# Performance work log

Hardware: AMD Instinct MI355X
Metric: run time of the kernel (lower is better)

The kernel has to match this reference:

```python
import jax, jax.numpy as jnp
import numpy as np

EMB_DIM = 256
HEAD_DIM = 32


def setup_inputs() -> dict:
    key = jax.random.key(0)
    kx, kq, kk, kv = jax.random.split(key, 4)
    B, S = 4, 4096
    x = jax.random.normal(kx, (B, S, EMB_DIM), dtype=jnp.float32)
    # Linear(emb_dim, head_dim, bias=False): store as [emb_dim, head_dim]
    sc = 1.0 / np.sqrt(EMB_DIM)
    Wq = jax.random.normal(kq, (EMB_DIM, HEAD_DIM), dtype=jnp.float32) * sc
    Wk = jax.random.normal(kk, (EMB_DIM, HEAD_DIM), dtype=jnp.float32) * sc
    Wv = jax.random.normal(kv, (EMB_DIM, HEAD_DIM), dtype=jnp.float32) * sc
    return {"x": x, "Wq": Wq, "Wk": Wk, "Wv": Wv}


def reference(x, Wq, Wk, Wv):
    # single-head attention with POST-softmax scaling (as in source).
    # Dropout treated as identity (eval mode) for determinism.
    scaling = HEAD_DIM ** (-0.5)
    q = jnp.einsum('bse,ed->bsd', x, Wq)
    k = jnp.einsum('bse,ed->bsd', x, Wk)
    v = jnp.einsum('bse,ed->bsd', x, Wv)
    energy = jnp.einsum('bqd,bkd->bqk', q, k)  # [B,S,S]
    att = jax.nn.softmax(energy, axis=-1) * scaling
    out = jnp.einsum('bqk,bkd->bqd', att, v)
    return out
```

## Files before the change

### kernel.cpp

```cpp
#include <hip/hip_runtime.h>

#define EMB 256
#define HD 32
#define SEQ 4096
#define NSPLIT 8
#define KRANGE 512
#define NT (KRANGE / 32)
#define NQROW 16384

typedef _Float16 half8 __attribute__((ext_vector_type(8)));
typedef _Float16 half4v __attribute__((ext_vector_type(4)));
typedef _Float16 half2v __attribute__((ext_vector_type(2)));
typedef float floatx4 __attribute__((ext_vector_type(4)));
typedef float floatx16 __attribute__((ext_vector_type(16)));
typedef unsigned uint2v __attribute__((ext_vector_type(2)));

#define L2E 1.44269504088896340736f
#define SCALING 0.17677669529663687f
#define DEFER_THR 8.0f

__device__ __forceinline__ half8 mk8(unsigned a, unsigned b, unsigned c, unsigned d) {
  union { unsigned u[4]; half8 h; } z;
  z.u[0] = a; z.u[1] = b; z.u[2] = c; z.u[3] = d;
  return z.h;
}

__device__ __forceinline__ void plswap(unsigned& a, unsigned& b) {
#if __has_builtin(__builtin_amdgcn_permlane32_swap)
  uint2v r = __builtin_amdgcn_permlane32_swap(a, b, false, false);
  a = r[0]; b = r[1];
#else
  unsigned sa = (unsigned)__shfl_xor((int)a, 32);
  unsigned sb = (unsigned)__shfl_xor((int)b, 32);
  bool hi = (threadIdx.x & 32) != 0;
  unsigned na = hi ? sb : a;
  unsigned nb = hi ? b : sa;
  a = na; b = nb;
#endif
}
__device__ __forceinline__ float plswap_red_max(float x) {
  return fmaxf(x, __shfl_xor(x, 32));
}
__device__ __forceinline__ float plswap_red_add(float x) {
  return x + __shfl_xor(x, 32);
}

__device__ __forceinline__ float sum2(unsigned pk, float acc) {
  half2v a = __builtin_bit_cast(half2v, pk);
#if __has_builtin(__builtin_amdgcn_fdot2)
  half2v one; one[0] = (_Float16)1.f; one[1] = (_Float16)1.f;
  return __builtin_amdgcn_fdot2(a, one, acc, false);
#else
  return acc + (float)a[0] + (float)a[1];
#endif
}

__global__ __launch_bounds__(256) void prep_kernel(const float* __restrict__ Wq,
                                                   const float* __restrict__ Wk,
                                                   const float* __restrict__ Wv,
                                                   _Float16* __restrict__ wsw) {
  int gid = blockIdx.x * 256 + threadIdx.x;
  int j    = gid & 7;
  int lane = (gid >> 3) & 63;
  int kc   = (gid >> 9) & 7;
  int half = (gid >> 12) & 1;
  int mat  = gid >> 13;
  const float* W = (mat == 0) ? Wq : ((mat == 1) ? Wk : Wv);
  int n = lane & 15, quad = lane >> 4;
  int e = kc * 32 + quad * 8 + j;
  int d = n + half * 16;
  float v = W[e * HD + d];
  if (mat == 0) v *= L2E;
  wsw[gid] = (_Float16)v;
}

__global__ __launch_bounds__(256) void qkv_kernel(const float* __restrict__ x,
                                                  const _Float16* __restrict__ wsw,
                                                  _Float16* __restrict__ qw,
                                                  _Float16* __restrict__ kw,
                                                  _Float16* __restrict__ vt2) {
  int lane = threadIdx.x & 63, wave = threadIdx.x >> 6;
  int n = lane & 15, quad = lane >> 4;
  int rowbase = blockIdx.x * 64 + wave * 16;

  floatx4 cq0 = {0,0,0,0}, cq1 = {0,0,0,0};
  floatx4 ck0 = {0,0,0,0}, ck1 = {0,0,0,0};
  floatx4 cv0 = {0,0,0,0}, cv1 = {0,0,0,0};

#pragma unroll
  for (int kc = 0; kc < 8; ++kc) {
    const float* xp = x + (rowbase + n) * EMB + kc * 32 + quad * 8;
    float4 xa = *(const float4*)(xp);
    float4 xb = *(const float4*)(xp + 4);
    half8 a;
    a[0] = (_Float16)xa.x; a[1] = (_Float16)xa.y; a[2] = (_Float16)xa.z; a[3] = (_Float16)xa.w;
    a[4] = (_Float16)xb.x; a[5] = (_Float16)xb.y; a[6] = (_Float16)xb.z; a[7] = (_Float16)xb.w;
    const _Float16* wp = wsw + (kc << 9) + (lane << 3);
    half8 bq0 = *(const half8*)(wp);
    half8 bq1 = *(const half8*)(wp + (8  << 9));
    half8 bk0 = *(const half8*)(wp + (16 << 9));
    half8 bk1 = *(const half8*)(wp + (24 << 9));
    half8 bv0 = *(const half8*)(wp + (32 << 9));
    half8 bv1 = *(const half8*)(wp + (40 << 9));
    cq0 = __builtin_amdgcn_mfma_f32_16x16x32_f16(a, bq0, cq0, 0, 0, 0);
    cq1 = __builtin_amdgcn_mfma_f32_16x16x32_f16(a, bq1, cq1, 0, 0, 0);
    ck0 = __builtin_amdgcn_mfma_f32_16x16x32_f16(a, bk0, ck0, 0, 0, 0);
    ck1 = __builtin_amdgcn_mfma_f32_16x16x32_f16(a, bk1, ck1, 0, 0, 0);
    cv0 = __builtin_amdgcn_mfma_f32_16x16x32_f16(a, bv0, cv0, 0, 0, 0);
    cv1 = __builtin_amdgcn_mfma_f32_16x16x32_f16(a, bv1, cv1, 0, 0, 0);
  }

  int b = rowbase >> 12;
  int s0 = rowbase & (SEQ - 1);
  _Float16* vbase = vt2 + (size_t)b * SEQ * HD;
#pragma unroll
  for (int r = 0; r < 4; ++r) {
    int row = rowbase + quad * 4 + r;
    qw[row * HD + n]      = (_Float16)cq0[r];
    qw[row * HD + n + 16] = (_Float16)cq1[r];
    kw[row * HD + n]      = (_Float16)ck0[r];
    kw[row * HD + n + 16] = (_Float16)ck1[r];
    int s = s0 + quad * 4 + r;
    int blk = (s >> 3) << 8, sl = s & 7;
    vbase[blk + n * 8 + sl]        = (_Float16)cv0[r];
    vbase[blk + (n + 16) * 8 + sl] = (_Float16)cv1[r];
  }
}

__global__ __launch_bounds__(256, 4) void attn_kernel(const _Float16* __restrict__ q,
                                                      const _Float16* __restrict__ k,
                                                      const _Float16* __restrict__ vt2,
                                                      _Float16* __restrict__ Op,
                                                      float* __restrict__ Mp,
                                                      float* __restrict__ Lp) {
  const int t = threadIdx.x;
  const int w = t >> 6, lane = t & 63;
  const int n2 = lane & 31, h = lane >> 5;
  const int qb = blockIdx.x & 127;
  const int sp = blockIdx.x >> 7;
  const int b = qb >> 5;
  const int qrow0 = qb * 128 + w * 32;
  const int key0 = sp * KRANGE;

  const _Float16* kb = k   + (size_t)(b * SEQ + key0) * HD;
  const _Float16* vb = vt2 + (size_t)b * SEQ * HD + (size_t)key0 * HD;

  half8 qf0 = *(const half8*)(q + (qrow0 + n2) * HD + h * 8);
  half8 qf1 = *(const half8*)(q + (qrow0 + n2) * HD + 16 + h * 8);

  floatx16 o;
#pragma unroll
  for (int r = 0; r < 16; ++r) o[r] = 0.f;
  const floatx16 zero16 = o;
  float m = -__builtin_huge_valf();
  float mtrue = -__builtin_huge_valf();
  float l = 0.f;

  half8 ka0 = *(const half8*)(kb + (size_t)n2 * HD + h * 8);
  half8 ka1 = *(const half8*)(kb + (size_t)n2 * HD + 16 + h * 8);
  half8 va0 = *(const half8*)(vb + h * 256 + n2 * 8);
  half8 va1 = *(const half8*)(vb + 512 + h * 256 + n2 * 8);

#pragma unroll 4
  for (int kt = 0; kt < NT; ++kt) {
    int nxt = (kt + 1) & (NT - 1);
    const _Float16* kn = kb + (size_t)(nxt * 32 + n2) * HD;
    const _Float16* vn = vb + nxt * 1024;
    half8 nka0 = *(const half8*)(kn + h * 8);
    half8 nka1 = *(const half8*)(kn + 16 + h * 8);
    half8 nva0 = *(const half8*)(vn + h * 256 + n2 * 8);
    half8 nva1 = *(const half8*)(vn + 512 + h * 256 + n2 * 8);

    floatx16 s = __builtin_amdgcn_mfma_f32_32x32x16_f16(ka0, qf0, zero16, 0, 0, 0);
    s = __builtin_amdgcn_mfma_f32_32x32x16_f16(ka1, qf1, s, 0, 0, 0);

    floatx4 s0 = {s[0], s[1], s[2], s[3]};
    floatx4 s1 = {s[4], s[5], s[6], s[7]};
    floatx4 s2 = {s[8], s[9], s[10], s[11]};
    floatx4 s3 = {s[12], s[13], s[14], s[15]};
    floatx4 t01 = __builtin_elementwise_max(s0, s1);
    floatx4 t23 = __builtin_elementwise_max(s2, s3);
    floatx4 t4  = __builtin_elementwise_max(t01, t23);
    float mm = fmaxf(fmaxf(t4[0], t4[1]), fmaxf(t4[2], t4[3]));
    mm = plswap_red_max(mm);
    mtrue = fmaxf(mtrue, mm);

    if (__any(mm > m + DEFER_THR)) {
      float mnew = fmaxf(m, mm);
      float alpha = __builtin_amdgcn_exp2f(m - mnew);
      m = mnew;
#pragma unroll
      for (int r = 0; r < 16; ++r) o[r] *= alpha;
      l *= alpha;
    }

    unsigned pk[8];
#pragma unroll
    for (int g = 0; g < 8; ++g) {
      float p0 = __builtin_amdgcn_exp2f(s[2 * g] - m);
      float p1 = __builtin_amdgcn_exp2f(s[2 * g + 1] - m);
      pk[g] = __builtin_bit_cast(unsigned, __builtin_amdgcn_cvt_pkrtz(p0, p1));
    }

    float lA = sum2(pk[3], sum2(pk[2], sum2(pk[1], sum2(pk[0], 0.f))));
    float lB = sum2(pk[7], sum2(pk[6], sum2(pk[5], sum2(pk[4], 0.f))));
    l += lA + lB;

    unsigned b00 = pk[0], b02 = pk[2]; plswap(b00, b02);
    unsigned b01 = pk[1], b03 = pk[3]; plswap(b01, b03);
    unsigned b10 = pk[4], b12 = pk[6]; plswap(b10, b12);
    unsigned b11 = pk[5], b13 = pk[7]; plswap(b11, b13);

    o = __builtin_amdgcn_mfma_f32_32x32x16_f16(va0, mk8(b00, b01, b02, b03), o, 0, 0, 0);
    o = __builtin_amdgcn_mfma_f32_32x32x16_f16(va1, mk8(b10, b11, b12, b13), o, 0, 0, 0);

    ka0 = nka0; ka1 = nka1; va0 = nva0; va1 = nva1;
  }

  float scale = __builtin_amdgcn_exp2f(m - mtrue);
  l *= scale;
  l = plswap_red_add(l);

  size_t obase = ((size_t)(sp * NQROW + qrow0) + n2) * 32;
#pragma unroll
  for (int bb = 0; bb < 4; ++bb) {
    half4v pv;
    pv[0] = (_Float16)(o[4 * bb + 0] * scale);
    pv[1] = (_Float16)(o[4 * bb + 1] * scale);
    pv[2] = (_Float16)(o[4 * bb + 2] * scale);
    pv[3] = (_Float16)(o[4 * bb + 3] * scale);
    *(half4v*)&Op[obase + 8 * bb + 4 * h] = pv;
  }
  if (h == 0) {
    int mi = sp * NQROW + qrow0 + n2;
    Mp[mi] = mtrue;
    Lp[mi] = l;
  }
}

__global__ __launch_bounds__(256) void combine_kernel(const _Float16* __restrict__ Op,
                                                      const float* __restrict__ Mp,
                                                      const float* __restrict__ Lp,
                                                      float* __restrict__ out) {
  int gid = blockIdx.x * 256 + threadIdx.x;
  int dc = gid & 7, qrow = gid >> 3;
  float mv[NSPLIT];
  float ms = -__builtin_huge_valf();
#pragma unroll
  for (int sp = 0; sp < NSPLIT; ++sp) {
    mv[sp] = Mp[sp * NQROW + qrow];
    ms = fmaxf(ms, mv[sp]);
  }
  float L = 0.f;
  floatx4 O = {0.f, 0.f, 0.f, 0.f};
#pragma unroll
  for (int sp = 0; sp < NSPLIT; ++sp) {
    float ww = __builtin_amdgcn_exp2f(mv[sp] - ms);
    L += ww * Lp[sp * NQROW + qrow];
    half4v ov = *(const half4v*)&Op[((size_t)(sp * NQROW + qrow)) * 32 + dc * 4];
#pragma unroll
    for (int r = 0; r < 4; ++r) O[r] += ww * (float)ov[r];
  }
  float inv = SCALING / L;
  floatx4 res = {O[0] * inv, O[1] * inv, O[2] * inv, O[3] * inv};
  *(floatx4*)&out[qrow * HD + dc * 4] = res;
}

extern "C" void kernel_launch(void* const* d_in, const int* in_sizes, int n_in,
                              void* d_out, int out_size, void* d_ws, size_t ws_size,
                              hipStream_t stream) {
  const float* x  = (const float*)d_in[0];
  const float* Wq = (const float*)d_in[1];
  const float* Wk = (const float*)d_in[2];
  const float* Wv = (const float*)d_in[3];
  float* out = (float*)d_out;

  _Float16* wsw = (_Float16*)d_ws;
  _Float16* qw  = wsw + 24576;
  _Float16* kw  = qw + NQROW * HD;
  _Float16* vt2 = kw + NQROW * HD;
  _Float16* Op  = vt2 + NQROW * HD;
  float* Mp = (float*)(Op + (size_t)NSPLIT * NQROW * 32);
  float* Lp = Mp + NSPLIT * NQROW;

  prep_kernel<<<96, 256, 0, stream>>>(Wq, Wk, Wv, wsw);
  qkv_kernel<<<256, 256, 0, stream>>>(x, wsw, qw, kw, vt2);
  attn_kernel<<<1024, 256, 0, stream>>>(qw, kw, vt2, Op, Mp, Lp);
  combine_kernel<<<512, 256, 0, stream>>>(Op, Mp, Lp, out);
}
```

Before: 98.13 us.

## Fuse weight prep into QKV and split-K combine into attention via counters

The weight swizzle/convert kernel is removed. Each QKV block now loads the three weight matrices, swizzles them and converts them to fp16 in shared memory (48KB LDS), and also zeroes a set of per-query-block counters. The separate combine kernel is removed. The last attention block to finish for a query block, detected with an atomic counter, merges the 8 split partials and writes the output. This cuts two launches and their gaps, at the cost of redundant weight prep in every QKV block, higher LDS use, and a tail in which a single block does the combine serially.

```diff
diff --git a/kernel.cpp b/kernel.cpp
--- a/kernel.cpp
+++ b/kernel.cpp
@@ -38,12 +38,6 @@
   a = na; b = nb;
 #endif
 }
-__device__ __forceinline__ float plswap_red_max(float x) {
-  return fmaxf(x, __shfl_xor(x, 32));
-}
-__device__ __forceinline__ float plswap_red_add(float x) {
-  return x + __shfl_xor(x, 32);
-}
 
 __device__ __forceinline__ float sum2(unsigned pk, float acc) {
   half2v a = __builtin_bit_cast(half2v, pk);
@@ -55,31 +49,40 @@
 #endif
 }
 
-__global__ __launch_bounds__(256) void prep_kernel(const float* __restrict__ Wq,
-                                                   const float* __restrict__ Wk,
-                                                   const float* __restrict__ Wv,
-                                                   _Float16* __restrict__ wsw) {
-  int gid = blockIdx.x * 256 + threadIdx.x;
-  int j    = gid & 7;
-  int lane = (gid >> 3) & 63;
-  int kc   = (gid >> 9) & 7;
-  int half = (gid >> 12) & 1;
-  int mat  = gid >> 13;
-  const float* W = (mat == 0) ? Wq : ((mat == 1) ? Wk : Wv);
-  int n = lane & 15, quad = lane >> 4;
-  int e = kc * 32 + quad * 8 + j;
-  int d = n + half * 16;
-  float v = W[e * HD + d];
-  if (mat == 0) v *= L2E;
-  wsw[gid] = (_Float16)v;
-}
-
 __global__ __launch_bounds__(256) void qkv_kernel(const float* __restrict__ x,
-                                                  const _Float16* __restrict__ wsw,
+                                                  const float* __restrict__ Wq,
+                                                  const float* __restrict__ Wk,
+                                                  const float* __restrict__ Wv,
                                                   _Float16* __restrict__ qw,
                                                   _Float16* __restrict__ kw,
-                                                  _Float16* __restrict__ vt2) {
-  int lane = threadIdx.x & 63, wave = threadIdx.x >> 6;
+                                                  _Float16* __restrict__ vt2,
+                                                  unsigned* __restrict__ cnt) {
+  __shared__ _Float16 wsl[24576];
+  const int tid = threadIdx.x;
+
+  if (blockIdx.x == 0 && tid < 128) cnt[tid] = 0;
+
+#pragma unroll
+  for (int i = 0; i < 24; ++i) {
+    const float* W = (i < 8) ? Wq : ((i < 16) ? Wk : Wv);
+    int lu = (i & 7) * 1024 + tid * 4;
+    float4 v4 = *(const float4*)(W + lu);
+    int e = lu >> 5;
+    int d0 = lu & 31;
+    int kc = e >> 5, quad = (e >> 3) & 3, j = e & 7;
+    int half = d0 >> 4;
+    int n0 = d0 & 15;
+    int mat = i >> 3;
+    int base = (((mat * 2 + half) * 8 + kc) << 9) + (quad << 7) + j;
+    float sc = (i < 8) ? L2E : 1.f;
+    wsl[base + (n0 + 0) * 8] = (_Float16)(v4.x * sc);
+    wsl[base + (n0 + 1) * 8] = (_Float16)(v4.y * sc);
+    wsl[base + (n0 + 2) * 8] = (_Float16)(v4.z * sc);
+    wsl[base + (n0 + 3) * 8] = (_Float16)(v4.w * sc);
+  }
+  __syncthreads();
+
+  int lane = tid & 63, wave = tid >> 6;
   int n = lane & 15, quad = lane >> 4;
   int rowbase = blockIdx.x * 64 + wave * 16;
 
@@ -89,13 +92,13 @@
 
 #pragma unroll
   for (int kc = 0; kc < 8; ++kc) {
-    const float* xp = x + (rowbase + n) * EMB + kc * 32 + quad * 8;
+    const float* xp = x + (size_t)(rowbase + n) * EMB + kc * 32 + quad * 8;
     float4 xa = *(const float4*)(xp);
     float4 xb = *(const float4*)(xp + 4);
     half8 a;
     a[0] = (_Float16)xa.x; a[1] = (_Float16)xa.y; a[2] = (_Float16)xa.z; a[3] = (_Float16)xa.w;
     a[4] = (_Float16)xb.x; a[5] = (_Float16)xb.y; a[6] = (_Float16)xb.z; a[7] = (_Float16)xb.w;
-    const _Float16* wp = wsw + (kc << 9) + (lane << 3);
+    const _Float16* wp = wsl + (kc << 9) + (lane << 3);
     half8 bq0 = *(const half8*)(wp);
     half8 bq1 = *(const half8*)(wp + (8  << 9));
     half8 bk0 = *(const half8*)(wp + (16 << 9));
@@ -132,7 +135,9 @@
                                                       const _Float16* __restrict__ vt2,
                                                       _Float16* __restrict__ Op,
                                                       float* __restrict__ Mp,
-                                                      float* __restrict__ Lp) {
+                                                      float* __restrict__ Lp,
+                                                      unsigned* __restrict__ cnt,
+                                                      float* __restrict__ out) {
   const int t = threadIdx.x;
   const int w = t >> 6, lane = t & 63;
   const int n2 = lane & 31, h = lane >> 5;
@@ -182,7 +187,7 @@
     floatx4 t23 = __builtin_elementwise_max(s2, s3);
     floatx4 t4  = __builtin_elementwise_max(t01, t23);
     float mm = fmaxf(fmaxf(t4[0], t4[1]), fmaxf(t4[2], t4[3]));
-    mm = plswap_red_max(mm);
+    mm = fmaxf(mm, __shfl_xor(mm, 32));
     mtrue = fmaxf(mtrue, mm);
 
     if (__any(mm > m + DEFER_THR)) {
@@ -219,7 +224,7 @@
 
   float scale = __builtin_amdgcn_exp2f(m - mtrue);
   l *= scale;
-  l = plswap_red_add(l);
+  l = l + __shfl_xor(l, 32);
 
   size_t obase = ((size_t)(sp * NQROW + qrow0) + n2) * 32;
 #pragma unroll
@@ -236,34 +241,44 @@
     Mp[mi] = mtrue;
     Lp[mi] = l;
   }
-}
-
-__global__ __launch_bounds__(256) void combine_kernel(const _Float16* __restrict__ Op,
-                                                      const float* __restrict__ Mp,
-                                                      const float* __restrict__ Lp,
-                                                      float* __restrict__ out) {
-  int gid = blockIdx.x * 256 + threadIdx.x;
-  int dc = gid & 7, qrow = gid >> 3;
-  float mv[NSPLIT];
-  float ms = -__builtin_huge_valf();
-#pragma unroll
-  for (int sp = 0; sp < NSPLIT; ++sp) {
-    mv[sp] = Mp[sp * NQROW + qrow];
-    ms = fmaxf(ms, mv[sp]);
-  }
-  float L = 0.f;
-  floatx4 O = {0.f, 0.f, 0.f, 0.f};
-#pragma unroll
-  for (int sp = 0; sp < NSPLIT; ++sp) {
-    float ww = __builtin_amdgcn_exp2f(mv[sp] - ms);
-    L += ww * Lp[sp * NQROW + qrow];
-    half4v ov = *(const half4v*)&Op[((size_t)(sp * NQROW + qrow)) * 32 + dc * 4];
-#pragma unroll
-    for (int r = 0; r < 4; ++r) O[r] += ww * (float)ov[r];
-  }
-  float inv = SCALING / L;
-  floatx4 res = {O[0] * inv, O[1] * inv, O[2] * inv, O[3] * inv};
-  *(floatx4*)&out[qrow * HD + dc * 4] = res;
+
+  __shared__ int lastflag;
+  __syncthreads();
+  if (t == 0) {
+    unsigned old = __hip_atomic_fetch_add(&cnt[qb], 1u, __ATOMIC_ACQ_REL,
+                                          __HIP_MEMORY_SCOPE_AGENT);
+    lastflag = (old == NSPLIT - 1u);
+  }
+  __syncthreads();
+  if (lastflag) {
+    __threadfence();
+#pragma unroll
+    for (int it = 0; it < 4; ++it) {
+      int item = it * 256 + t;
+      int qrow = qb * 128 + (item >> 3);
+      int dc = item & 7;
+      float mv[NSPLIT];
+      float ms = -__builtin_huge_valf();
+#pragma unroll
+      for (int sp2 = 0; sp2 < NSPLIT; ++sp2) {
+        mv[sp2] = Mp[sp2 * NQROW + qrow];
+        ms = fmaxf(ms, mv[sp2]);
+      }
+      float L = 0.f;
+      floatx4 O = {0.f, 0.f, 0.f, 0.f};
+#pragma unroll
+      for (int sp2 = 0; sp2 < NSPLIT; ++sp2) {
+        float ww = __builtin_amdgcn_exp2f(mv[sp2] - ms);
+        L += ww * Lp[sp2 * NQROW + qrow];
+        half4v ov = *(const half4v*)&Op[((size_t)(sp2 * NQROW + qrow)) * 32 + dc * 4];
+#pragma unroll
+        for (int r = 0; r < 4; ++r) O[r] += ww * (float)ov[r];
+      }
+      float inv = SCALING / L;
+      floatx4 res = {O[0] * inv, O[1] * inv, O[2] * inv, O[3] * inv};
+      *(floatx4*)&out[qrow * HD + dc * 4] = res;
+    }
+  }
 }
 
 extern "C" void kernel_launch(void* const* d_in, const int* in_sizes, int n_in,
@@ -275,16 +290,14 @@
   const float* Wv = (const float*)d_in[3];
   float* out = (float*)d_out;
 
-  _Float16* wsw = (_Float16*)d_ws;
-  _Float16* qw  = wsw + 24576;
+  _Float16* qw  = (_Float16*)d_ws;
   _Float16* kw  = qw + NQROW * HD;
   _Float16* vt2 = kw + NQROW * HD;
   _Float16* Op  = vt2 + NQROW * HD;
   float* Mp = (float*)(Op + (size_t)NSPLIT * NQROW * 32);
   float* Lp = Mp + NSPLIT * NQROW;
-
-  prep_kernel<<<96, 256, 0, stream>>>(Wq, Wk, Wv, wsw);
-  qkv_kernel<<<256, 256, 0, stream>>>(x, wsw, qw, kw, vt2);
-  attn_kernel<<<1024, 256, 0, stream>>>(qw, kw, vt2, Op, Mp, Lp);
-  combine_kernel<<<512, 256, 0, stream>>>(Op, Mp, Lp, out);
-}
+  unsigned* cnt = (unsigned*)(Lp + NSPLIT * NQROW);
+
+  qkv_kernel<<<256, 256, 0, stream>>>(x, Wq, Wk, Wv, qw, kw, vt2, cnt);
+  attn_kernel<<<1024, 256, 0, stream>>>(qw, kw, vt2, Op, Mp, Lp, cnt, out);
+}
```

Measured after the change: 142.4 us. 45.1% more time.
